# Optimization experiments

Hardware: AMD Instinct MI355X
Metric: run time of the kernel (lower is better)

Reference implementation:

```python
import jax, jax.numpy as jnp
import numpy as np

N = 50000
E = 800000
IN_DIM = 128
HID = 32
OUT = 64
H1, H2, H3 = 8, 8, 1
NEG_SLOPE = 0.2


def gatv2_layer(x, W, b, attn, src, dst, n_heads, d_out):
    # x: [N, F_in]; W: [F_in, n_heads*d_out]; attn: [n_heads, d_out]
    h = (x @ W + b).reshape(-1, n_heads, d_out)          # [N, H, D]
    e = jax.nn.leaky_relu(h[src] + h[dst], NEG_SLOPE)    # [E, H, D]
    score = jnp.einsum('ehd,hd->eh', e, attn)            # [E, H]
    m = jax.ops.segment_max(score, dst, num_segments=N)  # [N, H]
    ex = jnp.exp(score - m[dst])
    denom = jax.ops.segment_sum(ex, dst, num_segments=N)
    alpha = ex / denom[dst]                              # [E, H]
    out = jax.ops.segment_sum(alpha[:, :, None] * h[src], dst, num_segments=N)
    return out                                           # [N, H, D]


def setup_inputs() -> dict:
    key = jax.random.key(0)
    ks = jax.random.split(key, 12)
    x = jax.random.normal(ks[0], (N, IN_DIM), dtype=jnp.float32)
    src = jax.random.randint(ks[1], (E,), 0, N, dtype=jnp.int32)
    # ensure every node has at least one incoming edge (edge softmax well-defined)
    dst = jnp.concatenate([jnp.arange(N, dtype=jnp.int32),
                           jax.random.randint(ks[2], (E - N,), 0, N, dtype=jnp.int32)])

    def glorot(k, shape):
        fan_in, fan_out = shape[0], shape[1] if len(shape) > 1 else shape[0]
        s = jnp.sqrt(6.0 / (fan_in + fan_out)).astype(jnp.float32)
        return jax.random.uniform(k, shape, jnp.float32, -s, s)

    W1 = glorot(ks[3], (IN_DIM, H1 * HID)); b1 = jnp.zeros((H1 * HID,), jnp.float32)
    attn1 = glorot(ks[4], (H1, HID))
    W2 = glorot(ks[5], (H1 * HID, H2 * HID)); b2 = jnp.zeros((H2 * HID,), jnp.float32)
    attn2 = glorot(ks[6], (H2, HID))
    W3 = glorot(ks[7], (H2 * HID, H3 * OUT)); b3 = jnp.zeros((H3 * OUT,), jnp.float32)
    attn3 = glorot(ks[8], (H3, OUT))
    return {"x": x, "src": src, "dst": dst,
            "W1": W1, "b1": b1, "attn1": attn1,
            "W2": W2, "b2": b2, "attn2": attn2,
            "W3": W3, "b3": b3, "attn3": attn3}


def reference(x, src, dst, W1, b1, attn1, W2, b2, attn2, W3, b3, attn3):
    h = gatv2_layer(x, W1, b1, attn1, src, dst, H1, HID)
    h = jax.nn.elu(h).reshape(N, H1 * HID)               # activation + flatten(1)
    h = gatv2_layer(h, W2, b2, attn2, src, dst, H2, HID)
    h = jax.nn.elu(h).reshape(N, H2 * HID)
    h = gatv2_layer(h, W3, b3, attn3, src, dst, H3, OUT)
    logits = h.mean(axis=1)                              # mean over heads -> [N, OUT]
    return jnp.max(logits, axis=0)                       # graph max pooling -> [OUT]
```

## Files before the change

kernel.cpp:

```cpp
#include <hip/hip_runtime.h>
#include <hip/hip_bf16.h>

typedef unsigned int u32;
typedef unsigned short u16;
typedef _Float16 f16x2 __attribute__((ext_vector_type(2)));
typedef _Float16 f16x8 __attribute__((ext_vector_type(8)));
typedef float f32x4 __attribute__((ext_vector_type(4)));

#define NN 50000
#define EE 800000
#define SCAN_B ((NN + 255) / 256)
#define G1_TILES (((NN + 63) / 64) * 2)
#define CNT_B ((EE + 255) / 256)
#define A1_ROWS ((NN + 3) / 4)
#define F1_B 64
#define F1_PER ((A1_ROWS + F1_B - 1) / F1_B)

__device__ __forceinline__ f16x2 ash(u32 u) { union { u32 u; f16x2 h; } c; c.u = u; return c.h; }
__device__ __forceinline__ u32 h2u(f16x2 h) { union { u32 u; f16x2 h; } c; c.h = h; return c.u; }
__device__ __forceinline__ u16 f2h(float v) { _Float16 h = (_Float16)v; return *(u16*)&h; }
__device__ __forceinline__ u32 pack2h(float a, float b) {
    return (u32)f2h(a) | ((u32)f2h(b) << 16);
}
__device__ __forceinline__ float elu(float v) { return v > 0.f ? v : __expf(v) - 1.f; }


__global__ __launch_bounds__(256) void gat_prep_r26(const float* __restrict__ W1,
                                                    const float* __restrict__ W2,
                                                    const float* __restrict__ W3,
                                                    u16* __restrict__ W1t,
                                                    u16* __restrict__ W2t,
                                                    u16* __restrict__ W3t,
                                                    int* __restrict__ deg) {
    int b = blockIdx.x, t = threadIdx.x;
    if (b < 256) {
        if (t < 128) W1t[(long)b * 128 + t] = f2h(W1[(long)t * 256 + b]);
    } else if (b < 512) {
        int n = b - 256;
        W2t[(long)n * 256 + t] = f2h(W2[(long)t * 256 + n]);
    } else if (b < 576) {
        int n = b - 512;
        W3t[(long)n * 256 + t] = f2h(W3[(long)t * 64 + n]);
    } else {
        int i = (b - 576) * 256 + t;
        if (i < NN) deg[i] = 0;
    }
}


template <int AHF>
__device__ __forceinline__ void gemm128_body(const void* __restrict__ Ain,
                                             const u16* __restrict__ Wt,
                                             const float* __restrict__ bias,
                                             u16* __restrict__ C,
                                             int M, int K, int Nc,
                                             int bm, int bn) {
    __shared__ __align__(16) u16 As[64 * 40];
    __shared__ __align__(16) u16 Bs[128 * 40];
    const int t    = threadIdx.x;
    const int w    = t >> 6;
    const int lane = t & 63;
    const int sm   = t >> 2;
    const int sk   = (t & 3) * 8;
    const int fq   = (lane >> 4) * 8;
    const int fr   = lane & 15;
    const int nbase = w * 32;

    f32x4 acc[4][2] = {};

    for (int k0 = 0; k0 < K; k0 += 32) {
        {
            int gr = bm + sm;
            f16x8 av = {};
            if (gr < M) {
                if (AHF) {
                    av = *(const f16x8*)((const u16*)Ain + (long)gr * K + k0 + sk);
                } else {
                    const float* p = (const float*)Ain + (long)gr * K + k0 + sk;
                    #pragma unroll
                    for (int i = 0; i < 8; ++i) av[i] = (_Float16)p[i];
                }
            }
            *(f16x8*)&As[sm * 40 + sk] = av;
        }
        #pragma unroll
        for (int i = 0; i < 2; ++i) {
            int tau = t + i * 256;
            int row = tau >> 2, ck = (tau & 3) * 8;
            f16x8 bv = *(const f16x8*)(Wt + (long)(bn + row) * K + k0 + ck);
            *(f16x8*)&Bs[row * 40 + ck] = bv;
        }
        __syncthreads();
        f16x8 afr[4], bfr[2];
        #pragma unroll
        for (int mt = 0; mt < 4; ++mt)
            afr[mt] = *(const f16x8*)&As[(mt * 16 + fr) * 40 + fq];
        #pragma unroll
        for (int nt = 0; nt < 2; ++nt)
            bfr[nt] = *(const f16x8*)&Bs[(nbase + nt * 16 + fr) * 40 + fq];
        #pragma unroll
        for (int mt = 0; mt < 4; ++mt)
            #pragma unroll
            for (int nt = 0; nt < 2; ++nt)
                acc[mt][nt] = __builtin_amdgcn_mfma_f32_16x16x32_f16(
                    afr[mt], bfr[nt], acc[mt][nt], 0, 0, 0);
        __syncthreads();
    }
    #pragma unroll
    for (int mt = 0; mt < 4; ++mt) {
        #pragma unroll
        for (int r = 0; r < 4; ++r) {
            int row = bm + mt * 16 + (lane >> 4) * 4 + r;
            if (row >= M) continue;
            #pragma unroll
            for (int nt = 0; nt < 2; ++nt) {
                int col = bn + nbase + nt * 16 + fr;
                C[(long)row * Nc + col] = f2h(acc[mt][nt][r] + bias[col]);
            }
        }
    }
}


__global__ __launch_bounds__(256) void gat_fuse1_r26(const float* __restrict__ x,
                                                     const u16* __restrict__ W1t,
                                                     const float* __restrict__ b1,
                                                     u16* __restrict__ P,
                                                     const int* __restrict__ dst,
                                                     int* __restrict__ deg) {
    int b = blockIdx.x;
    if (b < G1_TILES) {
        int bm = (b >> 1) * 64;
        int bn = (b & 1) * 128;
        gemm128_body<0>(x, W1t, b1, P, NN, 128, 256, bm, bn);
    } else {
        int e = (b - G1_TILES) * 256 + threadIdx.x;
        if (e < EE) atomicAdd(&deg[dst[e]], 1);
    }
}


__global__ __launch_bounds__(256) void gat_gemm2_r26(const u16* __restrict__ Q,
                                                     const u16* __restrict__ W2t,
                                                     const float* __restrict__ b2,
                                                     u16* __restrict__ P) {
    __shared__ __align__(16) u16 As[64 * 40];
    __shared__ __align__(16) u16 Bs[256 * 40];
    const int t    = threadIdx.x;
    const int w    = t >> 6;
    const int lane = t & 63;
    const int sm   = t >> 2;
    const int sk   = (t & 3) * 8;
    const int fq   = (lane >> 4) * 8;
    const int fr   = lane & 15;
    const int nbase = w * 64;
    const int bm   = blockIdx.x * 64;

    f32x4 acc[4][4] = {};

    for (int k0 = 0; k0 < 256; k0 += 32) {
        {
            int gr = bm + sm;
            f16x8 av = {};
            if (gr < NN) av = *(const f16x8*)(Q + (long)gr * 256 + k0 + sk);
            *(f16x8*)&As[sm * 40 + sk] = av;
        }
        #pragma unroll
        for (int i = 0; i < 4; ++i) {
            int tau = t + i * 256;
            int row = tau >> 2, ck = (tau & 3) * 8;
            f16x8 bv = *(const f16x8*)(W2t + (long)row * 256 + k0 + ck);
            *(f16x8*)&Bs[row * 40 + ck] = bv;
        }
        __syncthreads();
        f16x8 afr[4], bfr[4];
        #pragma unroll
        for (int mt = 0; mt < 4; ++mt)
            afr[mt] = *(const f16x8*)&As[(mt * 16 + fr) * 40 + fq];
        #pragma unroll
        for (int nt = 0; nt < 4; ++nt)
            bfr[nt] = *(const f16x8*)&Bs[(nbase + nt * 16 + fr) * 40 + fq];
        #pragma unroll
        for (int mt = 0; mt < 4; ++mt)
            #pragma unroll
            for (int nt = 0; nt < 4; ++nt)
                acc[mt][nt] = __builtin_amdgcn_mfma_f32_16x16x32_f16(
                    afr[mt], bfr[nt], acc[mt][nt], 0, 0, 0);
        __syncthreads();
    }
    #pragma unroll
    for (int mt = 0; mt < 4; ++mt) {
        #pragma unroll
        for (int r = 0; r < 4; ++r) {
            int row = bm + mt * 16 + (lane >> 4) * 4 + r;
            if (row >= NN) continue;
            #pragma unroll
            for (int nt = 0; nt < 4; ++nt) {
                int col = nbase + nt * 16 + fr;
                P[(long)row * 256 + col] = f2h(acc[mt][nt][r] + b2[col]);
            }
        }
    }
}


__global__ __launch_bounds__(256) void gat_scana_r26(const int* __restrict__ deg,
                                                     int* __restrict__ bsum) {
    __shared__ int s[256];
    int t = threadIdx.x;
    int i = blockIdx.x * 256 + t;
    s[t] = (i < NN) ? deg[i] : 0;
    __syncthreads();
    for (int o = 128; o > 0; o >>= 1) {
        if (t < o) s[t] += s[t + o];
        __syncthreads();
    }
    if (t == 0) bsum[blockIdx.x] = s[0];
}

__global__ __launch_bounds__(256) void gat_scanc_r26(const int* __restrict__ deg,
                                                     const int* __restrict__ bsum,
                                                     int* __restrict__ row_ptr,
                                                     int* __restrict__ cursor) {
    __shared__ int sb[256];
    __shared__ int s[256];
    int t = threadIdx.x;
    sb[t] = (t < SCAN_B) ? bsum[t] : 0;
    __syncthreads();
    for (int o = 1; o < 256; o <<= 1) {
        int u = (t >= o) ? sb[t - o] : 0;
        __syncthreads();
        sb[t] += u;
        __syncthreads();
    }
    int boff = (blockIdx.x == 0) ? 0 : sb[blockIdx.x - 1];
    if (blockIdx.x == 0 && t == 0) row_ptr[NN] = sb[SCAN_B - 1];
    int i = blockIdx.x * 256 + t;
    int v = (i < NN) ? deg[i] : 0;
    s[t] = v;
    __syncthreads();
    for (int o = 1; o < 256; o <<= 1) {
        int u = (t >= o) ? s[t - o] : 0;
        __syncthreads();
        s[t] += u;
        __syncthreads();
    }
    if (i < NN) {
        int excl = s[t] - v + boff;
        row_ptr[i] = excl;
        cursor[i]  = excl;
    }
}

__global__ void gat_scatter_r26(const int* __restrict__ src, const int* __restrict__ dst,
                                int* __restrict__ cursor, int* __restrict__ esrc) {
    int e = blockIdx.x * 256 + threadIdx.x;
    if (e < EE) {
        int pos = atomicAdd(&cursor[dst[e]], 1);
        esrc[pos] = src[e];
    }
}


__global__ __launch_bounds__(256) void gat_gemm64_r26(const u16* __restrict__ Ain,
                                                      const u16* __restrict__ Wt,
                                                      const float* __restrict__ bias,
                                                      u16* __restrict__ C,
                                                      int M, int K, int Nc) {
    __shared__ __align__(16) u16 As[64 * 40];
    __shared__ __align__(16) u16 Bs[64 * 40];
    const int t    = threadIdx.x;
    const int bm   = blockIdx.x * 64;
    const int bn   = blockIdx.y * 64;
    const int w    = t >> 6;
    const int lane = t & 63;
    const int sm   = t >> 2;
    const int sk   = (t & 3) * 8;
    const int mbase = (w & 1) * 32;
    const int nbase = (w >> 1) * 32;
    const int fq    = (lane >> 4) * 8;
    const int fr    = lane & 15;

    f32x4 acc[2][2] = {};

    for (int k0 = 0; k0 < K; k0 += 32) {
        {
            int gr = bm + sm;
            f16x8 av = {};
            if (gr < M) av = *(const f16x8*)(Ain + (long)gr * K + k0 + sk);
            *(f16x8*)&As[sm * 40 + sk] = av;
        }
        {
            f16x8 bv = *(const f16x8*)(Wt + (long)(bn + sm) * K + k0 + sk);
            *(f16x8*)&Bs[sm * 40 + sk] = bv;
        }
        __syncthreads();
        f16x8 afr[2], bfr[2];
        #pragma unroll
        for (int mt = 0; mt < 2; ++mt)
            afr[mt] = *(const f16x8*)&As[(mbase + mt * 16 + fr) * 40 + fq];
        #pragma unroll
        for (int nt = 0; nt < 2; ++nt)
            bfr[nt] = *(const f16x8*)&Bs[(nbase + nt * 16 + fr) * 40 + fq];
        #pragma unroll
        for (int mt = 0; mt < 2; ++mt)
            #pragma unroll
            for (int nt = 0; nt < 2; ++nt)
                acc[mt][nt] = __builtin_amdgcn_mfma_f32_16x16x32_f16(
                    afr[mt], bfr[nt], acc[mt][nt], 0, 0, 0);
        __syncthreads();
    }
    #pragma unroll
    for (int mt = 0; mt < 2; ++mt) {
        #pragma unroll
        for (int r = 0; r < 4; ++r) {
            int row = bm + mbase + mt * 16 + (lane >> 4) * 4 + r;
            if (row >= M) continue;
            #pragma unroll
            for (int nt = 0; nt < 2; ++nt) {
                int col = bn + nbase + nt * 16 + fr;
                C[(long)row * Nc + col] = f2h(acc[mt][nt][r] + bias[col]);
            }
        }
    }
}


__global__ __launch_bounds__(256, 8) void gat_attn8_r26(const uint4* __restrict__ h4,
                                                        const int* __restrict__ row_ptr,
                                                        const int* __restrict__ esrc,
                                                        const float* __restrict__ attn,
                                                        uint4* __restrict__ act4) {
    int t = threadIdx.x;
    int lane = t & 63, wv = t >> 6;
    int hf = lane >> 5, sub = lane & 31;
    int li = lane & 7;
    int n = blockIdx.x * 4 + wv;
    float4 av0 = ((const float4*)attn)[sub * 2];
    float4 av1 = ((const float4*)attn)[sub * 2 + 1];
    f16x2 aw0 = {(_Float16)av0.x, (_Float16)av0.y};
    f16x2 aw1 = {(_Float16)av0.z, (_Float16)av0.w};
    f16x2 aw2 = {(_Float16)av1.x, (_Float16)av1.y};
    f16x2 aw3 = {(_Float16)av1.z, (_Float16)av1.w};
    const f16x2 c02 = {(_Float16)0.2f, (_Float16)0.2f};
    uint4 ud = h4[(long)n * 32 + sub];
    f16x2 hd0 = ash(ud.x), hd1 = ash(ud.y), hd2 = ash(ud.z), hd3 = ash(ud.w);
    int lo = __builtin_amdgcn_readfirstlane(row_ptr[n]);
    int hi = __builtin_amdgcn_readfirstlane(row_ptr[n + 1]);
    int clampv = hi - 1;
    float l = 0.f;
    f16x2 O0 = {}, O1 = {}, O2 = {}, O3 = {};
    int e = lo;
    int ia0 = lo + li;
    int myidx = esrc[ia0 < clampv ? ia0 : clampv];
    for (; e + 8 <= hi; e += 8) {
        int ia = e + 8 + li;
        int nextidx = esrc[ia < clampv ? ia : clampv];
        int srow[4];
        #pragma unroll
        for (int j2 = 0; j2 < 4; ++j2) srow[j2] = __shfl(myidx, 2 * j2 + hf, 8);
        uint4 u[4];
        #pragma unroll
        for (int j2 = 0; j2 < 4; ++j2) u[j2] = h4[(long)srow[j2] * 32 + sub];
        #pragma unroll
        for (int j2 = 0; j2 < 4; ++j2) {
            f16x2 x0 = ash(u[j2].x), x1 = ash(u[j2].y), x2 = ash(u[j2].z), x3 = ash(u[j2].w);
            f16x2 v0 = x0 + hd0, v1 = x1 + hd1, v2 = x2 + hd2, v3 = x3 + hd3;
            f16x2 r0 = __builtin_elementwise_max(v0, v0 * c02);
            f16x2 r1 = __builtin_elementwise_max(v1, v1 * c02);
            f16x2 r2 = __builtin_elementwise_max(v2, v2 * c02);
            f16x2 r3 = __builtin_elementwise_max(v3, v3 * c02);
            f16x2 acc = r0 * aw0;
            acc += r1 * aw1;
            acc += r2 * aw2;
            acc += r3 * aw3;
            float p = (float)acc.x + (float)acc.y;
            p += __shfl_xor(p, 1);
            p += __shfl_xor(p, 2);
            float w = __expf(p);
            l += w;
            _Float16 wh = (_Float16)w;
            f16x2 w2 = {wh, wh};
            O0 += x0 * w2; O1 += x1 * w2; O2 += x2 * w2; O3 += x3 * w2;
        }
        myidx = nextidx;
    }
    for (int j = 0; e + j < hi; j += 2) {
        int srow = __shfl(myidx, j + hf, 8);
        uint4 u = h4[(long)srow * 32 + sub];
        f16x2 x0 = ash(u.x), x1 = ash(u.y), x2 = ash(u.z), x3 = ash(u.w);
        f16x2 v0 = x0 + hd0, v1 = x1 + hd1, v2 = x2 + hd2, v3 = x3 + hd3;
        f16x2 r0 = __builtin_elementwise_max(v0, v0 * c02);
        f16x2 r1 = __builtin_elementwise_max(v1, v1 * c02);
        f16x2 r2 = __builtin_elementwise_max(v2, v2 * c02);
        f16x2 r3 = __builtin_elementwise_max(v3, v3 * c02);
        f16x2 acc = r0 * aw0;
        acc += r1 * aw1;
        acc += r2 * aw2;
        acc += r3 * aw3;
        float p = (float)acc.x + (float)acc.y;
        p += __shfl_xor(p, 1);
        p += __shfl_xor(p, 2);
        float w = (e + j + hf < hi) ? __expf(p) : 0.f;
        l += w;
        _Float16 wh = (_Float16)w;
        f16x2 w2 = {wh, wh};
        O0 += x0 * w2; O1 += x1 * w2; O2 += x2 * w2; O3 += x3 * w2;
    }
    l += __shfl_xor(l, 32);
    O0 += ash(__shfl_xor((int)h2u(O0), 32));
    O1 += ash(__shfl_xor((int)h2u(O1), 32));
    O2 += ash(__shfl_xor((int)h2u(O2), 32));
    O3 += ash(__shfl_xor((int)h2u(O3), 32));
    float rinv = 1.f / l;
    if (hf == 0) {
        uint4 outv;
        outv.x = pack2h(elu((float)O0.x * rinv), elu((float)O0.y * rinv));
        outv.y = pack2h(elu((float)O1.x * rinv), elu((float)O1.y * rinv));
        outv.z = pack2h(elu((float)O2.x * rinv), elu((float)O2.y * rinv));
        outv.w = pack2h(elu((float)O3.x * rinv), elu((float)O3.y * rinv));
        act4[(long)n * 32 + sub] = outv;
    }
}


__global__ __launch_bounds__(256) void gat_attn1_r26(const uint4* __restrict__ h4,
                                                     const int* __restrict__ row_ptr,
                                                     const int* __restrict__ esrc,
                                                     const float* __restrict__ attn,
                                                     float* __restrict__ blockmax) {
    int t = threadIdx.x;
    int lane = t & 63, wv = t >> 6;
    int g = lane >> 3, sub = lane & 7;
    int n = blockIdx.x * 4 + wv;
    float4 aq0 = ((const float4*)attn)[sub * 2];
    float4 aq1 = ((const float4*)attn)[sub * 2 + 1];
    f16x2 aw0 = {(_Float16)aq0.x, (_Float16)aq0.y};
    f16x2 aw1 = {(_Float16)aq0.z, (_Float16)aq0.w};
    f16x2 aw2 = {(_Float16)aq1.x, (_Float16)aq1.y};
    f16x2 aw3 = {(_Float16)aq1.z, (_Float16)aq1.w};
    const f16x2 c02 = {(_Float16)0.2f, (_Float16)0.2f};
    uint4 ud = h4[(long)n * 8 + sub];
    f16x2 hd0 = ash(ud.x), hd1 = ash(ud.y), hd2 = ash(ud.z), hd3 = ash(ud.w);
    int lo = row_ptr[n], hi = row_ptr[n + 1];
    float l = 0.f;
    f16x2 O0 = {}, O1 = {}, O2 = {}, O3 = {};
    int eg = lo + g;
    int s = esrc[(eg < hi) ? eg : hi - 1];
    uint4 ucur = h4[(long)s * 8 + sub];
    for (int e = lo; e < hi; e += 8) {
        int egn = e + 8 + g;
        int snext = esrc[(egn < hi) ? egn : hi - 1];
        bool more = (e + 8 < hi);
        uint4 unext = {};
        if (more) unext = h4[(long)snext * 8 + sub];
        bool valid = e + g < hi;
        f16x2 x0 = ash(ucur.x), x1 = ash(ucur.y), x2 = ash(ucur.z), x3 = ash(ucur.w);
        f16x2 v0 = x0 + hd0, v1 = x1 + hd1, v2 = x2 + hd2, v3 = x3 + hd3;
        f16x2 r0 = __builtin_elementwise_max(v0, v0 * c02);
        f16x2 r1 = __builtin_elementwise_max(v1, v1 * c02);
        f16x2 r2 = __builtin_elementwise_max(v2, v2 * c02);
        f16x2 r3 = __builtin_elementwise_max(v3, v3 * c02);
        f16x2 acc = r0 * aw0;
        acc += r1 * aw1;
        acc += r2 * aw2;
        acc += r3 * aw3;
        float p = (float)acc.x + (float)acc.y;
        p += __shfl_xor(p, 1);
        p += __shfl_xor(p, 2);
        p += __shfl_xor(p, 4);
        float w = valid ? __expf(p) : 0.f;
        l += w;
        _Float16 wh = (_Float16)w;
        f16x2 w2 = {wh, wh};
        O0 += x0 * w2; O1 += x1 * w2; O2 += x2 * w2; O3 += x3 * w2;
        if (more) ucur = unext;
    }
    l += __shfl_xor(l, 8); l += __shfl_xor(l, 16); l += __shfl_xor(l, 32);
    O0 += ash(__shfl_xor((int)h2u(O0), 8));
    O0 += ash(__shfl_xor((int)h2u(O0), 16));
    O0 += ash(__shfl_xor((int)h2u(O0), 32));
    O1 += ash(__shfl_xor((int)h2u(O1), 8));
    O1 += ash(__shfl_xor((int)h2u(O1), 16));
    O1 += ash(__shfl_xor((int)h2u(O1), 32));
    O2 += ash(__shfl_xor((int)h2u(O2), 8));
    O2 += ash(__shfl_xor((int)h2u(O2), 16));
    O2 += ash(__shfl_xor((int)h2u(O2), 32));
    O3 += ash(__shfl_xor((int)h2u(O3), 8));
    O3 += ash(__shfl_xor((int)h2u(O3), 16));
    O3 += ash(__shfl_xor((int)h2u(O3), 32));
    float rinv = 1.f / l;
    __shared__ float sm[4][64];
    if (g == 0) {
        sm[wv][sub * 8 + 0] = (float)O0.x * rinv; sm[wv][sub * 8 + 1] = (float)O0.y * rinv;
        sm[wv][sub * 8 + 2] = (float)O1.x * rinv; sm[wv][sub * 8 + 3] = (float)O1.y * rinv;
        sm[wv][sub * 8 + 4] = (float)O2.x * rinv; sm[wv][sub * 8 + 5] = (float)O2.y * rinv;
        sm[wv][sub * 8 + 6] = (float)O3.x * rinv; sm[wv][sub * 8 + 7] = (float)O3.y * rinv;
    }
    __syncthreads();
    if (wv == 0) {
        float r = sm[0][lane];
        #pragma unroll
        for (int i = 1; i < 4; ++i) r = fmaxf(r, sm[i][lane]);
        blockmax[(long)blockIdx.x * 64 + lane] = r;
    }
}


__global__ __launch_bounds__(256) void gat_final1_r26(const float* __restrict__ blockmax,
                                                      float* __restrict__ partial) {
    int t = threadIdx.x;
    int lane = t & 63, wv = t >> 6;
    int r0 = blockIdx.x * F1_PER;
    int r1 = r0 + F1_PER; if (r1 > A1_ROWS) r1 = A1_ROWS;
    float v = -1e30f;
    for (int r = r0 + wv; r < r1; r += 4)
        v = fmaxf(v, blockmax[(long)r * 64 + lane]);
    __shared__ float sm[4][64];
    sm[wv][lane] = v;
    __syncthreads();
    if (wv == 0) {
        float r = sm[0][lane];
        #pragma unroll
        for (int i = 1; i < 4; ++i) r = fmaxf(r, sm[i][lane]);
        partial[(long)blockIdx.x * 64 + lane] = r;
    }
}

__global__ __launch_bounds__(256) void gat_final2_r26(const float* __restrict__ partial,
                                                      float* __restrict__ out) {
    int t = threadIdx.x;
    int lane = t & 63, wv = t >> 6;
    float v = -1e30f;
    for (int r = wv; r < F1_B; r += 4)
        v = fmaxf(v, partial[(long)r * 64 + lane]);
    __shared__ float sm[4][64];
    sm[wv][lane] = v;
    __syncthreads();
    if (wv == 0) {
        float r = sm[0][lane];
        #pragma unroll
        for (int i = 1; i < 4; ++i) r = fmaxf(r, sm[i][lane]);
        out[lane] = r;
    }
}


extern "C" void kernel_launch(void* const* d_in, const int* in_sizes, int n_in,
                              void* d_out, int out_size, void* d_ws, size_t ws_size,
                              hipStream_t stream) {
    const float* x     = (const float*)d_in[0];
    const int*   src   = (const int*)  d_in[1];
    const int*   dst   = (const int*)  d_in[2];
    const float* W1    = (const float*)d_in[3];
    const float* b1    = (const float*)d_in[4];
    const float* attn1 = (const float*)d_in[5];
    const float* W2    = (const float*)d_in[6];
    const float* b2    = (const float*)d_in[7];
    const float* attn2 = (const float*)d_in[8];
    const float* W3    = (const float*)d_in[9];
    const float* b3    = (const float*)d_in[10];
    const float* attn3 = (const float*)d_in[11];
    float* out = (float*)d_out;

    char* ws = (char*)d_ws;
    size_t off = 0;
    auto carve = [&](size_t bytes) { void* p = ws + off; off += (bytes + 255) & ~size_t(255); return p; };
    u16*   P        = (u16*)  carve((size_t)NN * 256 * 2);
    u16*   Q        = (u16*)  carve((size_t)NN * 256 * 2);
    u16*   h3       = (u16*)  carve((size_t)NN * 64 * 2);
    int*   row_ptr  = (int*)  carve((size_t)(NN + 1) * 4);
    int*   deg      = (int*)  carve((size_t)NN * 4);
    int*   cursor   = (int*)  carve((size_t)NN * 4);
    int*   esrc     = (int*)  carve((size_t)EE * 4);
    float* blockmax = (float*)carve((size_t)A1_ROWS * 64 * 4);
    float* partial  = (float*)carve((size_t)F1_B * 64 * 4);
    int*   bsum     = (int*)  carve((size_t)SCAN_B * 4);
    u16*   W1t      = (u16*)  carve((size_t)256 * 128 * 2);
    u16*   W2t      = (u16*)  carve((size_t)256 * 256 * 2);
    u16*   W3t      = (u16*)  carve((size_t)64 * 256 * 2);

    gat_prep_r26<<<576 + SCAN_B, 256, 0, stream>>>(W1, W2, W3, W1t, W2t, W3t, deg);
    gat_fuse1_r26<<<G1_TILES + CNT_B, 256, 0, stream>>>(x, W1t, b1, P, dst, deg);
    gat_scana_r26<<<SCAN_B, 256, 0, stream>>>(deg, bsum);
    gat_scanc_r26<<<SCAN_B, 256, 0, stream>>>(deg, bsum, row_ptr, cursor);
    gat_scatter_r26<<<CNT_B, 256, 0, stream>>>(src, dst, cursor, esrc);

    gat_attn8_r26<<<NN / 4, 256, 0, stream>>>((const uint4*)P, row_ptr, esrc, attn1, (uint4*)Q);

    gat_gemm2_r26<<<(NN + 63) / 64, 256, 0, stream>>>(Q, W2t, b2, P);
    gat_attn8_r26<<<NN / 4, 256, 0, stream>>>((const uint4*)P, row_ptr, esrc, attn2, (uint4*)Q);

    gat_gemm64_r26<<<dim3((NN + 63) / 64, 1), 256, 0, stream>>>(Q, W3t, b3, h3, NN, 256, 64);
    gat_attn1_r26<<<A1_ROWS, 256, 0, stream>>>((const uint4*)h3, row_ptr, esrc, attn3, blockmax);

    gat_final1_r26<<<F1_B, 256, 0, stream>>>(blockmax, partial);
    gat_final2_r26<<<1, 256, 0, stream>>>(partial, out);
}
```

Measured before the change: 363.1 us.

## Order attention waves by node in-degree buckets to balance per-block work

Builds a degree histogram (capped at 63) during the CSR scan, prefix-sums it in a tiny kernel, and scatters node ids into a degree-sorted order array. The three attention kernels then pick their node from this order, so the four waves in a block handle nodes of similar in-degree. This is meant to cut wave imbalance and divergence inside blocks. In exchange it adds a kernel launch, an atomic counting pass, and indirect node indexing that reduces output write locality. It also drops the unused half-precision input template path from the GEMM helper.

```diff
diff --git a/kernel.cpp b/kernel.cpp
--- a/kernel.cpp
+++ b/kernel.cpp
@@ -25,13 +25,14 @@
 __device__ __forceinline__ float elu(float v) { return v > 0.f ? v : __expf(v) - 1.f; }
 
 
-__global__ __launch_bounds__(256) void gat_prep_r26(const float* __restrict__ W1,
+__global__ __launch_bounds__(256) void gat_prep_r28(const float* __restrict__ W1,
                                                     const float* __restrict__ W2,
                                                     const float* __restrict__ W3,
                                                     u16* __restrict__ W1t,
                                                     u16* __restrict__ W2t,
                                                     u16* __restrict__ W3t,
-                                                    int* __restrict__ deg) {
+                                                    int* __restrict__ deg,
+                                                    int* __restrict__ bucket) {
     int b = blockIdx.x, t = threadIdx.x;
     if (b < 256) {
         if (t < 128) W1t[(long)b * 128 + t] = f2h(W1[(long)t * 256 + b]);
@@ -44,12 +45,12 @@
     } else {
         int i = (b - 576) * 256 + t;
         if (i < NN) deg[i] = 0;
-    }
-}
-
-
-template <int AHF>
-__device__ __forceinline__ void gemm128_body(const void* __restrict__ Ain,
+        if (b == 576 && t < 64) bucket[t] = 0;
+    }
+}
+
+
+__device__ __forceinline__ void gemm128_body(const float* __restrict__ Ain,
                                              const u16* __restrict__ Wt,
                                              const float* __restrict__ bias,
                                              u16* __restrict__ C,
@@ -73,13 +74,9 @@
             int gr = bm + sm;
             f16x8 av = {};
             if (gr < M) {
-                if (AHF) {
-                    av = *(const f16x8*)((const u16*)Ain + (long)gr * K + k0 + sk);
-                } else {
-                    const float* p = (const float*)Ain + (long)gr * K + k0 + sk;
-                    #pragma unroll
-                    for (int i = 0; i < 8; ++i) av[i] = (_Float16)p[i];
-                }
+                const float* p = Ain + (long)gr * K + k0 + sk;
+                #pragma unroll
+                for (int i = 0; i < 8; ++i) av[i] = (_Float16)p[i];
             }
             *(f16x8*)&As[sm * 40 + sk] = av;
         }
@@ -122,7 +119,7 @@
 }
 
 
-__global__ __launch_bounds__(256) void gat_fuse1_r26(const float* __restrict__ x,
+__global__ __launch_bounds__(256) void gat_fuse1_r28(const float* __restrict__ x,
                                                      const u16* __restrict__ W1t,
                                                      const float* __restrict__ b1,
                                                      u16* __restrict__ P,
@@ -132,7 +129,7 @@
     if (b < G1_TILES) {
         int bm = (b >> 1) * 64;
         int bn = (b & 1) * 128;
-        gemm128_body<0>(x, W1t, b1, P, NN, 128, 256, bm, bn);
+        gemm128_body(x, W1t, b1, P, NN, 128, 256, bm, bn);
     } else {
         int e = (b - G1_TILES) * 256 + threadIdx.x;
         if (e < EE) atomicAdd(&deg[dst[e]], 1);
@@ -140,7 +137,7 @@
 }
 
 
-__global__ __launch_bounds__(256) void gat_gemm2_r26(const u16* __restrict__ Q,
+__global__ __launch_bounds__(256) void gat_gemm2_r28(const u16* __restrict__ Q,
                                                      const u16* __restrict__ W2t,
                                                      const float* __restrict__ b2,
                                                      u16* __restrict__ P) {
@@ -204,7 +201,7 @@
 }
 
 
-__global__ __launch_bounds__(256) void gat_scana_r26(const int* __restrict__ deg,
+__global__ __launch_bounds__(256) void gat_scana_r28(const int* __restrict__ deg,
                                                      int* __restrict__ bsum) {
     __shared__ int s[256];
     int t = threadIdx.x;
@@ -218,10 +215,11 @@
     if (t == 0) bsum[blockIdx.x] = s[0];
 }
 
-__global__ __launch_bounds__(256) void gat_scanc_r26(const int* __restrict__ deg,
+__global__ __launch_bounds__(256) void gat_scanc_r28(const int* __restrict__ deg,
                                                      const int* __restrict__ bsum,
                                                      int* __restrict__ row_ptr,
-                                                     int* __restrict__ cursor) {
+                                                     int* __restrict__ cursor,
+                                                     int* __restrict__ bucket) {
     __shared__ int sb[256];
     __shared__ int s[256];
     int t = threadIdx.x;
@@ -249,20 +247,47 @@
         int excl = s[t] - v + boff;
         row_ptr[i] = excl;
         cursor[i]  = excl;
-    }
-}
-
-__global__ void gat_scatter_r26(const int* __restrict__ src, const int* __restrict__ dst,
-                                int* __restrict__ cursor, int* __restrict__ esrc) {
-    int e = blockIdx.x * 256 + threadIdx.x;
-    if (e < EE) {
-        int pos = atomicAdd(&cursor[dst[e]], 1);
-        esrc[pos] = src[e];
-    }
-}
-
-
-__global__ __launch_bounds__(256) void gat_gemm64_r26(const u16* __restrict__ Ain,
+        int d = v < 63 ? v : 63;
+        atomicAdd(&bucket[d], 1);
+    }
+}
+
+__global__ __launch_bounds__(64) void gat_bscan_r28(const int* __restrict__ bucket,
+                                                    int* __restrict__ boff) {
+    int t = threadIdx.x;
+    int v = bucket[t];
+    int s = v;
+    #pragma unroll
+    for (int o = 1; o < 64; o <<= 1) {
+        int u = __shfl_up(s, o);
+        if (t >= o) s += u;
+    }
+    boff[t] = s - v;
+}
+
+__global__ void gat_scatter_r28(const int* __restrict__ src, const int* __restrict__ dst,
+                                int* __restrict__ cursor, int* __restrict__ esrc,
+                                const int* __restrict__ deg, int* __restrict__ boff,
+                                int* __restrict__ ord) {
+    int b = blockIdx.x;
+    if (b < CNT_B) {
+        int e = b * 256 + threadIdx.x;
+        if (e < EE) {
+            int pos = atomicAdd(&cursor[dst[e]], 1);
+            esrc[pos] = src[e];
+        }
+    } else {
+        int i = (b - CNT_B) * 256 + threadIdx.x;
+        if (i < NN) {
+            int d = deg[i]; d = d < 63 ? d : 63;
+            int pos = atomicAdd(&boff[d], 1);
+            ord[pos] = i;
+        }
+    }
+}
+
+
+__global__ __launch_bounds__(256) void gat_gemm64_r28(const u16* __restrict__ Ain,
                                                       const u16* __restrict__ Wt,
                                                       const float* __restrict__ bias,
                                                       u16* __restrict__ C,
@@ -326,16 +351,17 @@
 }
 
 
-__global__ __launch_bounds__(256, 8) void gat_attn8_r26(const uint4* __restrict__ h4,
+__global__ __launch_bounds__(256, 8) void gat_attn8_r28(const uint4* __restrict__ h4,
                                                         const int* __restrict__ row_ptr,
                                                         const int* __restrict__ esrc,
                                                         const float* __restrict__ attn,
-                                                        uint4* __restrict__ act4) {
+                                                        uint4* __restrict__ act4,
+                                                        const int* __restrict__ ord) {
     int t = threadIdx.x;
     int lane = t & 63, wv = t >> 6;
     int hf = lane >> 5, sub = lane & 31;
     int li = lane & 7;
-    int n = blockIdx.x * 4 + wv;
+    int n = ord[blockIdx.x * 4 + wv];
     float4 av0 = ((const float4*)attn)[sub * 2];
     float4 av1 = ((const float4*)attn)[sub * 2 + 1];
     f16x2 aw0 = {(_Float16)av0.x, (_Float16)av0.y};
@@ -424,15 +450,16 @@
 }
 
 
-__global__ __launch_bounds__(256) void gat_attn1_r26(const uint4* __restrict__ h4,
+__global__ __launch_bounds__(256) void gat_attn1_r28(const uint4* __restrict__ h4,
                                                      const int* __restrict__ row_ptr,
                                                      const int* __restrict__ esrc,
                                                      const float* __restrict__ attn,
-                                                     float* __restrict__ blockmax) {
+                                                     float* __restrict__ blockmax,
+                                                     const int* __restrict__ ord) {
     int t = threadIdx.x;
     int lane = t & 63, wv = t >> 6;
     int g = lane >> 3, sub = lane & 7;
-    int n = blockIdx.x * 4 + wv;
+    int n = ord[blockIdx.x * 4 + wv];
     float4 aq0 = ((const float4*)attn)[sub * 2];
     float4 aq1 = ((const float4*)attn)[sub * 2 + 1];
     f16x2 aw0 = {(_Float16)aq0.x, (_Float16)aq0.y};
@@ -507,7 +534,7 @@
 }
 
 
-__global__ __launch_bounds__(256) void gat_final1_r26(const float* __restrict__ blockmax,
+__global__ __launch_bounds__(256) void gat_final1_r28(const float* __restrict__ blockmax,
                                                       float* __restrict__ partial) {
     int t = threadIdx.x;
     int lane = t & 63, wv = t >> 6;
@@ -527,7 +554,7 @@
     }
 }
 
-__global__ __launch_bounds__(256) void gat_final2_r26(const float* __restrict__ partial,
+__global__ __launch_bounds__(256) void gat_final2_r28(const float* __restrict__ partial,
                                                       float* __restrict__ out) {
     int t = threadIdx.x;
     int lane = t & 63, wv = t >> 6;
@@ -573,27 +600,31 @@
     int*   deg      = (int*)  carve((size_t)NN * 4);
     int*   cursor   = (int*)  carve((size_t)NN * 4);
     int*   esrc     = (int*)  carve((size_t)EE * 4);
+    int*   ord      = (int*)  carve((size_t)NN * 4);
     float* blockmax = (float*)carve((size_t)A1_ROWS * 64 * 4);
     float* partial  = (float*)carve((size_t)F1_B * 64 * 4);
     int*   bsum     = (int*)  carve((size_t)SCAN_B * 4);
+    int*   bucket   = (int*)  carve((size_t)64 * 4);
+    int*   boff     = (int*)  carve((size_t)64 * 4);
     u16*   W1t      = (u16*)  carve((size_t)256 * 128 * 2);
     u16*   W2t      = (u16*)  carve((size_t)256 * 256 * 2);
     u16*   W3t      = (u16*)  carve((size_t)64 * 256 * 2);
 
-    gat_prep_r26<<<576 + SCAN_B, 256, 0, stream>>>(W1, W2, W3, W1t, W2t, W3t, deg);
-    gat_fuse1_r26<<<G1_TILES + CNT_B, 256, 0, stream>>>(x, W1t, b1, P, dst, deg);
-    gat_scana_r26<<<SCAN_B, 256, 0, stream>>>(deg, bsum);
-    gat_scanc_r26<<<SCAN_B, 256, 0, stream>>>(deg, bsum, row_ptr, cursor);
-    gat_scatter_r26<<<CNT_B, 256, 0, stream>>>(src, dst, cursor, esrc);
-
-    gat_attn8_r26<<<NN / 4, 256, 0, stream>>>((const uint4*)P, row_ptr, esrc, attn1, (uint4*)Q);
-
-    gat_gemm2_r26<<<(NN + 63) / 64, 256, 0, stream>>>(Q, W2t, b2, P);
-    gat_attn8_r26<<<NN / 4, 256, 0, stream>>>((const uint4*)P, row_ptr, esrc, attn2, (uint4*)Q);
-
-    gat_gemm64_r26<<<dim3((NN + 63) / 64, 1), 256, 0, stream>>>(Q, W3t, b3, h3, NN, 256, 64);
-    gat_attn1_r26<<<A1_ROWS, 256, 0, stream>>>((const uint4*)h3, row_ptr, esrc, attn3, blockmax);
-
-    gat_final1_r26<<<F1_B, 256, 0, stream>>>(blockmax, partial);
-    gat_final2_r26<<<1, 256, 0, stream>>>(partial, out);
-}
+    gat_prep_r28<<<576 + SCAN_B, 256, 0, stream>>>(W1, W2, W3, W1t, W2t, W3t, deg, bucket);
+    gat_fuse1_r28<<<G1_TILES + CNT_B, 256, 0, stream>>>(x, W1t, b1, P, dst, deg);
+    gat_scana_r28<<<SCAN_B, 256, 0, stream>>>(deg, bsum);
+    gat_scanc_r28<<<SCAN_B, 256, 0, stream>>>(deg, bsum, row_ptr, cursor, bucket);
+    gat_bscan_r28<<<1, 64, 0, stream>>>(bucket, boff);
+    gat_scatter_r28<<<CNT_B + SCAN_B, 256, 0, stream>>>(src, dst, cursor, esrc, deg, boff, ord);
+
+    gat_attn8_r28<<<NN / 4, 256, 0, stream>>>((const uint4*)P, row_ptr, esrc, attn1, (uint4*)Q, ord);
+
+    gat_gemm2_r28<<<(NN + 63) / 64, 256, 0, stream>>>(Q, W2t, b2, P);
+    gat_attn8_r28<<<NN / 4, 256, 0, stream>>>((const uint4*)P, row_ptr, esrc, attn2, (uint4*)Q, ord);
+
+    gat_gemm64_r28<<<dim3((NN + 63) / 64, 1), 256, 0, stream>>>(Q, W3t, b3, h3, NN, 256, 64);
+    gat_attn1_r28<<<A1_ROWS, 256, 0, stream>>>((const uint4*)h3, row_ptr, esrc, attn3, blockmax, ord);
+
+    gat_final1_r28<<<F1_B, 256, 0, stream>>>(blockmax, partial);
+    gat_final2_r28<<<1, 256, 0, stream>>>(partial, out);
+}
```

Result: slower. 629.7 us (+73.4%).
